# Kernel tuning notes

Measured on AMD Instinct MI355X. Metric: run time of the kernel, lower is better.

The kernel has to match this reference:

```python
import jax, jax.numpy as jnp
import numpy as np

ITEM_NUM = 50000
TARGET_ITEM_NUM = 50000
EMB = 128
N_LAYERS = 3
N_EDGES = 800000
N_NODES = ITEM_NUM + 1  # forward uses item_emb[:item_num+1]


def gcn_conv(x, row, col, W, b, n):
    """PyG GCNConv: symmetric-normalized aggregation with self-loops.
    out = D^{-1/2} (A + I) D^{-1/2} (x @ W) + b
    """
    h = x @ W  # [n, d]
    loops = jnp.arange(n)
    r = jnp.concatenate([row, loops])  # source
    c = jnp.concatenate([col, loops])  # target
    deg = jax.ops.segment_sum(jnp.ones(r.shape[0], x.dtype), c, num_segments=n)
    dinv = jnp.where(deg > 0, deg ** -0.5, jnp.zeros_like(deg))
    norm = dinv[r] * dinv[c]  # [E+n]
    out = jax.ops.segment_sum(h[r] * norm[:, None], c, num_segments=n)
    return out + b


def setup_inputs() -> dict:
    key = jax.random.key(0)
    k0, k1, k2 = jax.random.split(key, 3)
    edge_index = jax.random.randint(k0, (2, N_EDGES), 0, N_NODES)
    total = ITEM_NUM + TARGET_ITEM_NUM + 1
    # xavier_uniform for embedding table and per-layer GCN weights
    lim_e = float(np.sqrt(6.0 / (total + EMB)))
    item_emb = jax.random.uniform(k1, (total, EMB), jnp.float32, -lim_e, lim_e)
    lim_w = float(np.sqrt(6.0 / (EMB + EMB)))
    W = jax.random.uniform(k2, (N_LAYERS, EMB, EMB), jnp.float32, -lim_w, lim_w)
    b = jnp.zeros((N_LAYERS, EMB), jnp.float32)
    return {"edge_index": edge_index, "item_emb": item_emb, "W": W, "b": b}


def reference(edge_index, item_emb, W, b):
    n = N_NODES
    row, col = edge_index[0], edge_index[1]
    embeds = [item_emb[:n]]
    for i in range(N_LAYERS):
        embeds.append(gcn_conv(embeds[-1], row, col, W[i], b[i], n))
    return sum(embeds)  # [n, EMB], sum over layer embeddings
```

## Files before the change

### kernel.cpp

```cpp
#include <hip/hip_runtime.h>
#include <hip/hip_bf16.h>


constexpr int NN   = 50001;
constexpr int D    = 128;
constexpr int NPAD = 50048;
constexpr int NBK  = 196;
constexpr int CAP  = 7680;
constexpr int ZROW = NPAD - 1;

using bf16x8 = __attribute__((ext_vector_type(8))) short;
using f32x4  = __attribute__((ext_vector_type(4))) float;
using u16x8  = __attribute__((ext_vector_type(8))) unsigned short;
using u32x4  = __attribute__((ext_vector_type(4))) unsigned;

__device__ __forceinline__ ushort f2b(float f) {
    unsigned u = __float_as_uint(f);
    return (ushort)((u + 0x7FFFu + ((u >> 16) & 1u)) >> 16);
}
__device__ __forceinline__ float b2f(ushort u) {
    return __uint_as_float((unsigned)u << 16);
}

__global__ __launch_bounds__(256)
void k_build(const int* __restrict__ row, const int* __restrict__ col,
             int* __restrict__ partCur, unsigned* __restrict__ part,
             const float* __restrict__ W, ushort* __restrict__ Wt, int E) {
    int b = blockIdx.x, t = threadIdx.x;
    if (b < NBK) {
        __shared__ int hist[256];
        __shared__ int base[256];
        hist[t] = 0;
        __syncthreads();
        int e0 = b * 4096;
        unsigned rec[16];
        int bkt[16];
#pragma unroll
        for (int k = 0; k < 16; k++) {
            int e = e0 + k * 256 + t;
            if (e < E) {
                int r = row[e], c = col[e];
                rec[k] = (unsigned)r | ((unsigned)(c & 255) << 16);
                bkt[k] = c >> 8;
                atomicAdd(&hist[bkt[k]], 1);
            } else bkt[k] = -1;
        }
        __syncthreads();
        if (hist[t] > 0) base[t] = t * CAP + atomicAdd(&partCur[t], hist[t]);
        __syncthreads();
#pragma unroll
        for (int k = 0; k < 16; k++) {
            if (bkt[k] >= 0) {
                int pos = atomicAdd(&base[bkt[k]], 1);
                if (pos < (bkt[k] + 1) * CAP) part[pos] = rec[k];
            }
        }
    } else {
        int idx = (b - NBK) * 256 + t;
        int l = idx >> 14, rem = idx & 16383;
        int c = rem >> 7, k = rem & 127;
        Wt[idx] = f2b(W[l * D * D + k * D + c]);
    }
}

__global__ __launch_bounds__(256)
void k_scat(const unsigned* __restrict__ part, const int* __restrict__ partCur,
            float* __restrict__ dinv, unsigned* __restrict__ rp,
            ushort* __restrict__ meta, int n) {
    __shared__ int hist[256];
    __shared__ int sm[256];
    __shared__ int off[256];
    __shared__ int cur[256];
    int b = blockIdx.x, t = threadIdx.x;
    int node0 = b * 256;
    int nn = min(256, n - node0);
    int T = min(partCur[b], CAP);
    const unsigned* pb = part + (size_t)b * CAP;
    hist[t] = 0;
    __syncthreads();
    for (int i = t; i < T; i += 256) atomicAdd(&hist[pb[i] >> 16], 1);
    __syncthreads();
    int v = hist[t];
    int pv = (v + 15) & ~15;
    sm[t] = pv;
    __syncthreads();
    for (int ofs = 1; ofs < 256; ofs <<= 1) {
        int u = (t >= ofs) ? sm[t - ofs] : 0;
        __syncthreads();
        sm[t] += u;
        __syncthreads();
    }
    off[t] = sm[t] - pv;
    cur[t] = 0;
    if (t < nn) {
        dinv[node0 + t] = rsqrtf((float)v + 1.0f);
        rp[node0 + t] = (unsigned)(b * CAP + off[t]) | ((unsigned)v << 21);
    }
    __syncthreads();
    for (int i = t; i < T; i += 256) {
        unsigned rec = pb[i];
        int dl = (int)(rec >> 16);
        int pos = off[dl] + atomicAdd(&cur[dl], 1);
        if (pos < CAP) meta[(size_t)b * CAP + pos] = (ushort)(rec & 0xFFFFu);
    }
    int base = off[t];
    for (int p = v; p < pv; p++)
        if (base + p < CAP) meta[(size_t)b * CAP + base + p] = (ushort)ZROW;
}

constexpr int WT_LD = 136;
__global__ __launch_bounds__(256)
void k_gemm0(const float* __restrict__ emb, const ushort* __restrict__ WtL,
             const float* __restrict__ dinv, ushort* __restrict__ h, int n) {
    __shared__ ushort wlds[D * WT_LD];
    for (int idx = threadIdx.x; idx < D * (D / 8); idx += 256) {
        int r = idx >> 4, c8 = (idx & 15) * 8;
        *(uint4*)&wlds[r * WT_LD + c8] = *(const uint4*)&WtL[r * D + c8];
    }
    __syncthreads();

    int wave = threadIdx.x >> 6, lane = threadIdx.x & 63;
    int q = lane >> 4, i = lane & 15;
    int waveRow = blockIdx.x * 128 + wave * 32;

    bf16x8 a[2][4];
#pragma unroll
    for (int rt = 0; rt < 2; rt++) {
        const float* base = emb + (size_t)(waveRow + rt * 16 + i) * D + q * 8;
#pragma unroll
        for (int ks = 0; ks < 4; ks++) {
            float4 v0 = *(const float4*)(base + ks * 32);
            float4 v1 = *(const float4*)(base + ks * 32 + 4);
            bf16x8 aa;
            aa[0] = (short)f2b(v0.x); aa[1] = (short)f2b(v0.y);
            aa[2] = (short)f2b(v0.z); aa[3] = (short)f2b(v0.w);
            aa[4] = (short)f2b(v1.x); aa[5] = (short)f2b(v1.y);
            aa[6] = (short)f2b(v1.z); aa[7] = (short)f2b(v1.w);
            a[rt][ks] = aa;
        }
    }

    f32x4 acc[2][8] = {};
#pragma unroll
    for (int ct = 0; ct < 8; ct++) {
        const ushort* wbase = &wlds[(ct * 16 + i) * WT_LD + q * 8];
#pragma unroll
        for (int ks = 0; ks < 4; ks++) {
            bf16x8 bfr = *(const bf16x8*)(wbase + ks * 32);
            acc[0][ct] = __builtin_amdgcn_mfma_f32_16x16x32_bf16(a[0][ks], bfr, acc[0][ct], 0, 0, 0);
            acc[1][ct] = __builtin_amdgcn_mfma_f32_16x16x32_bf16(a[1][ks], bfr, acc[1][ct], 0, 0, 0);
        }
    }

#pragma unroll
    for (int rt = 0; rt < 2; rt++)
#pragma unroll
        for (int r4 = 0; r4 < 4; r4++) {
            int row = waveRow + rt * 16 + q * 4 + r4;
            float dv = (row < n) ? dinv[row] : 0.f;
#pragma unroll
            for (int ct = 0; ct < 8; ct++)
                h[(size_t)row * D + ct * 16 + i] = f2b(acc[rt][ct][r4] * dv);
        }
}

__global__ __launch_bounds__(256)
void k_fused(const unsigned* __restrict__ rp, const ushort* __restrict__ meta,
             const ushort* __restrict__ h_in,
             const float* __restrict__ dinv, const float* __restrict__ bias,
             const ushort* __restrict__ Wn,
             ushort* __restrict__ xb_out, ushort* __restrict__ h_out, int n) {
    __shared__ ushort xlds[16 * WT_LD];
    __shared__ float  sdinv[16];
    int tid  = threadIdx.x;
    int nl   = tid >> 4;
    int l    = tid & 15;
    int node0 = blockIdx.x * 16;
    int node  = node0 + nl;

    u16x8 w = {0, 0, 0, 0, 0, 0, 0, 0};
    float di = 0.f;
    if (node < n) {
        unsigned pk = rp[node];
        int s   = (int)(pk & 0x1FFFFFu);
        int deg = (int)(pk >> 21);
        const ushort* hl = h_in + (l << 3);

        u32x4 sv = *(const u32x4*)(hl + (size_t)node * D);
        di = dinv[node];
        const float4* bp = (const float4*)(bias + (l << 3));
        float4 b0 = bp[0], b1 = bp[1];

        float accL[4], accH[4];
#pragma unroll
        for (int k = 0; k < 4; k++) {
            accL[k] = __uint_as_float(sv[k] << 16);
            accH[k] = __uint_as_float(sv[k] & 0xFFFF0000u);
        }
        for (int j = 0; j < deg; j += 16) {
            u16x8 m0 = *(const u16x8*)&meta[s + j];
            u16x8 m1 = *(const u16x8*)&meta[s + j + 8];
            u32x4 v[16];
#pragma unroll
            for (int u = 0; u < 8; u++) v[u]     = *(const u32x4*)(hl + (size_t)m0[u] * D);
#pragma unroll
            for (int u = 0; u < 8; u++) v[8 + u] = *(const u32x4*)(hl + (size_t)m1[u] * D);
#pragma unroll
            for (int u = 0; u < 16; u++)
#pragma unroll
                for (int k = 0; k < 4; k++) {
                    accL[k] += __uint_as_float(v[u][k] << 16);
                    accH[k] += __uint_as_float(v[u][k] & 0xFFFF0000u);
                }
        }
        w[0] = f2b(fmaf(accL[0], di, b0.x));
        w[1] = f2b(fmaf(accH[0], di, b0.y));
        w[2] = f2b(fmaf(accL[1], di, b0.z));
        w[3] = f2b(fmaf(accH[1], di, b0.w));
        w[4] = f2b(fmaf(accL[2], di, b1.x));
        w[5] = f2b(fmaf(accH[2], di, b1.y));
        w[6] = f2b(fmaf(accL[3], di, b1.z));
        w[7] = f2b(fmaf(accH[3], di, b1.w));
        *(u16x8*)(xb_out + (size_t)node * D + (l << 3)) = w;
    }
    *(u16x8*)&xlds[nl * WT_LD + l * 8] = w;
    if (l == 0) sdinv[nl] = di;
    __syncthreads();

    int wave = tid >> 6, lane = tid & 63;
    int q = lane >> 4, i = lane & 15;

    bf16x8 a[4];
#pragma unroll
    for (int ks = 0; ks < 4; ks++)
        a[ks] = *(const bf16x8*)&xlds[i * WT_LD + ks * 32 + q * 8];

    f32x4 acc[2] = {};
#pragma unroll
    for (int ct = 0; ct < 2; ct++) {
        const ushort* wbase = &Wn[(size_t)(wave * 32 + ct * 16 + i) * D + q * 8];
#pragma unroll
        for (int ks = 0; ks < 4; ks++) {
            bf16x8 bfr = *(const bf16x8*)(wbase + ks * 32);
            acc[ct] = __builtin_amdgcn_mfma_f32_16x16x32_bf16(a[ks], bfr, acc[ct], 0, 0, 0);
        }
    }

#pragma unroll
    for (int r4 = 0; r4 < 4; r4++) {
        int rr = q * 4 + r4;
        float dv = sdinv[rr];
#pragma unroll
        for (int ct = 0; ct < 2; ct++)
            h_out[(size_t)(node0 + rr) * D + wave * 32 + ct * 16 + i] =
                f2b(acc[ct][r4] * dv);
    }
}

__global__ __launch_bounds__(256)
void k_pull_final(const unsigned* __restrict__ rp, const ushort* __restrict__ meta,
                  const ushort* __restrict__ h,
                  const float* __restrict__ dinv, const float* __restrict__ bias,
                  const float* __restrict__ emb, const ushort* __restrict__ x1,
                  const ushort* __restrict__ x2, float* __restrict__ out, int n) {
    int node = blockIdx.x * 16 + (threadIdx.x >> 4);
    int l    = threadIdx.x & 15;
    if (node >= n) return;
    unsigned pk = rp[node];
    int s   = (int)(pk & 0x1FFFFFu);
    int deg = (int)(pk >> 21);
    size_t o = (size_t)node * D + (l << 3);
    const ushort* hl = h + (l << 3);

    u32x4 sv = *(const u32x4*)(hl + (size_t)node * D);
    float di = dinv[node];
    const float4* bp = (const float4*)(bias + (l << 3));
    float4 b0 = bp[0], b1 = bp[1];
    const float4* ep = (const float4*)(emb + o);
    float4 e0 = ep[0], e1 = ep[1];
    u16x8 w1 = *(const u16x8*)(x1 + o);
    u16x8 w2 = *(const u16x8*)(x2 + o);

    float accL[4], accH[4];
#pragma unroll
    for (int k = 0; k < 4; k++) {
        accL[k] = __uint_as_float(sv[k] << 16);
        accH[k] = __uint_as_float(sv[k] & 0xFFFF0000u);
    }
    for (int j = 0; j < deg; j += 16) {
        u16x8 m0 = *(const u16x8*)&meta[s + j];
        u16x8 m1 = *(const u16x8*)&meta[s + j + 8];
        u32x4 v[16];
#pragma unroll
        for (int u = 0; u < 8; u++) v[u]     = *(const u32x4*)(hl + (size_t)m0[u] * D);
#pragma unroll
        for (int u = 0; u < 8; u++) v[8 + u] = *(const u32x4*)(hl + (size_t)m1[u] * D);
#pragma unroll
        for (int u = 0; u < 16; u++)
#pragma unroll
            for (int k = 0; k < 4; k++) {
                accL[k] += __uint_as_float(v[u][k] << 16);
                accH[k] += __uint_as_float(v[u][k] & 0xFFFF0000u);
            }
    }
    f32x4 o0, o1;
    o0[0] = e0.x + b2f(w1[0]) + b2f(w2[0]) + fmaf(accL[0], di, b0.x);
    o0[1] = e0.y + b2f(w1[1]) + b2f(w2[1]) + fmaf(accH[0], di, b0.y);
    o0[2] = e0.z + b2f(w1[2]) + b2f(w2[2]) + fmaf(accL[1], di, b0.z);
    o0[3] = e0.w + b2f(w1[3]) + b2f(w2[3]) + fmaf(accH[1], di, b0.w);
    o1[0] = e1.x + b2f(w1[4]) + b2f(w2[4]) + fmaf(accL[2], di, b1.x);
    o1[1] = e1.y + b2f(w1[5]) + b2f(w2[5]) + fmaf(accH[2], di, b1.y);
    o1[2] = e1.z + b2f(w1[6]) + b2f(w2[6]) + fmaf(accL[3], di, b1.z);
    o1[3] = e1.w + b2f(w1[7]) + b2f(w2[7]) + fmaf(accH[3], di, b1.w);
    __builtin_nontemporal_store(o0, (f32x4*)(out + o));
    __builtin_nontemporal_store(o1, (f32x4*)(out + o) + 1);
}

extern "C" void kernel_launch(void* const* d_in, const int* in_sizes, int n_in,
                              void* d_out, int out_size, void* d_ws, size_t ws_size,
                              hipStream_t stream) {
    const int*   edge = (const int*)d_in[0];
    const float* emb  = (const float*)d_in[1];
    const float* W    = (const float*)d_in[2];
    const float* b    = (const float*)d_in[3];
    float* out = (float*)d_out;

    const int E = in_sizes[0] / 2;
    const int n = NN;
    const int* row = edge;
    const int* col = edge + E;

    char* ws = (char*)d_ws;
    size_t off = 0;
    auto carve = [&](size_t bytes) { char* p = ws + off; off = (off + bytes + 511) / 512 * 512; return p; };
    int*      partCur = (int*)     carve(256 * 4);
    unsigned* part    = (unsigned*)carve((size_t)NBK * CAP * 4);
    ushort*   meta    = (ushort*)  carve((size_t)NBK * CAP * 2);
    unsigned* rp      = (unsigned*)carve((size_t)n * 4);
    float*    dinv    = (float*)   carve((size_t)n * 4);
    ushort*   Wt      = (ushort*)  carve((size_t)3 * D * D * 2);
    ushort*   xb1     = (ushort*)  carve((size_t)NPAD * D * 2);
    ushort*   xb2     = (ushort*)  carve((size_t)NPAD * D * 2);
    ushort*   hA      = (ushort*)  carve((size_t)NPAD * D * 2);
    ushort*   hB      = (ushort*)  carve((size_t)NPAD * D * 2);

    (void)hipMemsetAsync(partCur, 0, 256 * 4, stream);

    const int build_blocks = NBK + 192;
    k_build<<<build_blocks, 256, 0, stream>>>(row, col, partCur, part, W, Wt, E);
    k_scat <<<NBK, 256, 0, stream>>>(part, partCur, dinv, rp, meta, n);

    const int gemm_blocks  = NPAD / 128;
    const int fused_blocks = NPAD / 16;
    const int final_blocks = (n + 15) / 16;

    k_gemm0<<<gemm_blocks, 256, 0, stream>>>(emb, Wt, dinv, hA, n);
    k_fused<<<fused_blocks, 256, 0, stream>>>(rp, meta, hA, dinv, b,
                                              Wt + (size_t)1 * D * D, xb1, hB, n);
    k_fused<<<fused_blocks, 256, 0, stream>>>(rp, meta, hB, dinv, b + D,
                                              Wt + (size_t)2 * D * D, xb2, hA, n);
    k_pull_final<<<final_blocks, 256, 0, stream>>>(rp, meta, hA, dinv, b + 2 * D,
                                                   emb, xb1, xb2, out, n);
}
```

Baseline: 243.0 us.

## Fold layer-0 GEMM into the graph-build kernel and move dinv scaling into gather

The first-layer GEMM (emb @ W0) no longer depends on dinv, so it now runs inside the edge-bucketing prep kernel as extra blocks, which removes one launch and lets the GEMM overlap with the partitioning. Layer 1's aggregation therefore scales each gathered neighbour row by its dinv (an extra per-edge dinv load and FMA), and the self term is scaled by di. dinv is padded to NPAD with zeros so ZROW padding indices stay valid. The cost is extra random dinv reads in the first fused pass and a larger shared-memory footprint in the prep kernel.

```diff
diff --git a/kernel.cpp b/kernel.cpp
--- a/kernel.cpp
+++ b/kernel.cpp
@@ -8,6 +8,7 @@
 constexpr int NBK  = 196;
 constexpr int CAP  = 7680;
 constexpr int ZROW = NPAD - 1;
+constexpr int GB   = NPAD / 128;
 
 using bf16x8 = __attribute__((ext_vector_type(8))) short;
 using f32x4  = __attribute__((ext_vector_type(4))) float;
@@ -22,17 +23,77 @@
     return __uint_as_float((unsigned)u << 16);
 }
 
+constexpr int WT_LD = 136;
+
 __global__ __launch_bounds__(256)
-void k_build(const int* __restrict__ row, const int* __restrict__ col,
-             int* __restrict__ partCur, unsigned* __restrict__ part,
-             const float* __restrict__ W, ushort* __restrict__ Wt, int E) {
+void k_prep(const int* __restrict__ row, const int* __restrict__ col,
+            int* __restrict__ partCur, unsigned* __restrict__ part,
+            const float* __restrict__ W, ushort* __restrict__ Wt,
+            const float* __restrict__ emb, ushort* __restrict__ h,
+            int E, int n) {
+    __shared__ ushort wlds[D * WT_LD];
     int b = blockIdx.x, t = threadIdx.x;
-    if (b < NBK) {
-        __shared__ int hist[256];
-        __shared__ int base[256];
+
+    if (b < GB) {
+        for (int i4 = t; i4 < D * (D / 4); i4 += 256) {
+            int k = i4 >> 5, c4 = (i4 & 31) * 4;
+            float4 v = ((const float4*)W)[i4];
+            wlds[(c4 + 0) * WT_LD + k] = f2b(v.x);
+            wlds[(c4 + 1) * WT_LD + k] = f2b(v.y);
+            wlds[(c4 + 2) * WT_LD + k] = f2b(v.z);
+            wlds[(c4 + 3) * WT_LD + k] = f2b(v.w);
+        }
+        __syncthreads();
+
+        int wave = t >> 6, lane = t & 63;
+        int q = lane >> 4, i = lane & 15;
+        int waveRow = b * 128 + wave * 32;
+
+        bf16x8 a[2][4];
+#pragma unroll
+        for (int rt = 0; rt < 2; rt++) {
+            const float* base = emb + (size_t)(waveRow + rt * 16 + i) * D + q * 8;
+#pragma unroll
+            for (int ks = 0; ks < 4; ks++) {
+                float4 v0 = *(const float4*)(base + ks * 32);
+                float4 v1 = *(const float4*)(base + ks * 32 + 4);
+                bf16x8 aa;
+                aa[0] = (short)f2b(v0.x); aa[1] = (short)f2b(v0.y);
+                aa[2] = (short)f2b(v0.z); aa[3] = (short)f2b(v0.w);
+                aa[4] = (short)f2b(v1.x); aa[5] = (short)f2b(v1.y);
+                aa[6] = (short)f2b(v1.z); aa[7] = (short)f2b(v1.w);
+                a[rt][ks] = aa;
+            }
+        }
+
+        f32x4 acc[2][8] = {};
+#pragma unroll
+        for (int ct = 0; ct < 8; ct++) {
+            const ushort* wbase = &wlds[(ct * 16 + i) * WT_LD + q * 8];
+#pragma unroll
+            for (int ks = 0; ks < 4; ks++) {
+                bf16x8 bfr = *(const bf16x8*)(wbase + ks * 32);
+                acc[0][ct] = __builtin_amdgcn_mfma_f32_16x16x32_bf16(a[0][ks], bfr, acc[0][ct], 0, 0, 0);
+                acc[1][ct] = __builtin_amdgcn_mfma_f32_16x16x32_bf16(a[1][ks], bfr, acc[1][ct], 0, 0, 0);
+            }
+        }
+
+#pragma unroll
+        for (int rt = 0; rt < 2; rt++)
+#pragma unroll
+            for (int r4 = 0; r4 < 4; r4++) {
+                int r = waveRow + rt * 16 + q * 4 + r4;
+#pragma unroll
+                for (int ct = 0; ct < 8; ct++)
+                    h[(size_t)r * D + ct * 16 + i] =
+                        (r < n) ? f2b(acc[rt][ct][r4]) : (ushort)0;
+            }
+    } else if (b < GB + NBK) {
+        int* hist = (int*)wlds;
+        int* base = hist + 256;
         hist[t] = 0;
         __syncthreads();
-        int e0 = b * 4096;
+        int e0 = (b - GB) * 4096;
         unsigned rec[16];
         int bkt[16];
 #pragma unroll
@@ -56,10 +117,10 @@
             }
         }
     } else {
-        int idx = (b - NBK) * 256 + t;
-        int l = idx >> 14, rem = idx & 16383;
+        int idx = (b - GB - NBK) * 256 + t;
+        int l = 1 + (idx >> 14), rem = idx & 16383;
         int c = rem >> 7, k = rem & 127;
-        Wt[idx] = f2b(W[l * D * D + k * D + c]);
+        Wt[(size_t)16384 + idx] = f2b(W[l * D * D + k * D + c]);
     }
 }
 
@@ -95,6 +156,8 @@
     if (t < nn) {
         dinv[node0 + t] = rsqrtf((float)v + 1.0f);
         rp[node0 + t] = (unsigned)(b * CAP + off[t]) | ((unsigned)v << 21);
+    } else if (node0 + t < NPAD) {
+        dinv[node0 + t] = 0.f;
     }
     __syncthreads();
     for (int i = t; i < T; i += 256) {
@@ -108,62 +171,7 @@
         if (base + p < CAP) meta[(size_t)b * CAP + base + p] = (ushort)ZROW;
 }
 
-constexpr int WT_LD = 136;
-__global__ __launch_bounds__(256)
-void k_gemm0(const float* __restrict__ emb, const ushort* __restrict__ WtL,
-             const float* __restrict__ dinv, ushort* __restrict__ h, int n) {
-    __shared__ ushort wlds[D * WT_LD];
-    for (int idx = threadIdx.x; idx < D * (D / 8); idx += 256) {
-        int r = idx >> 4, c8 = (idx & 15) * 8;
-        *(uint4*)&wlds[r * WT_LD + c8] = *(const uint4*)&WtL[r * D + c8];
-    }
-    __syncthreads();
-
-    int wave = threadIdx.x >> 6, lane = threadIdx.x & 63;
-    int q = lane >> 4, i = lane & 15;
-    int waveRow = blockIdx.x * 128 + wave * 32;
-
-    bf16x8 a[2][4];
-#pragma unroll
-    for (int rt = 0; rt < 2; rt++) {
-        const float* base = emb + (size_t)(waveRow + rt * 16 + i) * D + q * 8;
-#pragma unroll
-        for (int ks = 0; ks < 4; ks++) {
-            float4 v0 = *(const float4*)(base + ks * 32);
-            float4 v1 = *(const float4*)(base + ks * 32 + 4);
-            bf16x8 aa;
-            aa[0] = (short)f2b(v0.x); aa[1] = (short)f2b(v0.y);
-            aa[2] = (short)f2b(v0.z); aa[3] = (short)f2b(v0.w);
-            aa[4] = (short)f2b(v1.x); aa[5] = (short)f2b(v1.y);
-            aa[6] = (short)f2b(v1.z); aa[7] = (short)f2b(v1.w);
-            a[rt][ks] = aa;
-        }
-    }
-
-    f32x4 acc[2][8] = {};
-#pragma unroll
-    for (int ct = 0; ct < 8; ct++) {
-        const ushort* wbase = &wlds[(ct * 16 + i) * WT_LD + q * 8];
-#pragma unroll
-        for (int ks = 0; ks < 4; ks++) {
-            bf16x8 bfr = *(const bf16x8*)(wbase + ks * 32);
-            acc[0][ct] = __builtin_amdgcn_mfma_f32_16x16x32_bf16(a[0][ks], bfr, acc[0][ct], 0, 0, 0);
-            acc[1][ct] = __builtin_amdgcn_mfma_f32_16x16x32_bf16(a[1][ks], bfr, acc[1][ct], 0, 0, 0);
-        }
-    }
-
-#pragma unroll
-    for (int rt = 0; rt < 2; rt++)
-#pragma unroll
-        for (int r4 = 0; r4 < 4; r4++) {
-            int row = waveRow + rt * 16 + q * 4 + r4;
-            float dv = (row < n) ? dinv[row] : 0.f;
-#pragma unroll
-            for (int ct = 0; ct < 8; ct++)
-                h[(size_t)row * D + ct * 16 + i] = f2b(acc[rt][ct][r4] * dv);
-        }
-}
-
+template <int SCALED>
 __global__ __launch_bounds__(256)
 void k_fused(const unsigned* __restrict__ rp, const ushort* __restrict__ meta,
              const ushort* __restrict__ h_in,
@@ -191,11 +199,12 @@
         const float4* bp = (const float4*)(bias + (l << 3));
         float4 b0 = bp[0], b1 = bp[1];
 
+        float selfs = SCALED ? 1.f : di;
         float accL[4], accH[4];
 #pragma unroll
         for (int k = 0; k < 4; k++) {
-            accL[k] = __uint_as_float(sv[k] << 16);
-            accH[k] = __uint_as_float(sv[k] & 0xFFFF0000u);
+            accL[k] = selfs * __uint_as_float(sv[k] << 16);
+            accH[k] = selfs * __uint_as_float(sv[k] & 0xFFFF0000u);
         }
         for (int j = 0; j < deg; j += 16) {
             u16x8 m0 = *(const u16x8*)&meta[s + j];
@@ -205,12 +214,20 @@
             for (int u = 0; u < 8; u++) v[u]     = *(const u32x4*)(hl + (size_t)m0[u] * D);
 #pragma unroll
             for (int u = 0; u < 8; u++) v[8 + u] = *(const u32x4*)(hl + (size_t)m1[u] * D);
+            float dv[16];
+            if constexpr (!SCALED) {
+#pragma unroll
+                for (int u = 0; u < 8; u++) { dv[u] = dinv[m0[u]]; dv[8 + u] = dinv[m1[u]]; }
+            }
 #pragma unroll
             for (int u = 0; u < 16; u++)
 #pragma unroll
                 for (int k = 0; k < 4; k++) {
-                    accL[k] += __uint_as_float(v[u][k] << 16);
-                    accH[k] += __uint_as_float(v[u][k] & 0xFFFF0000u);
+                    float lo = __uint_as_float(v[u][k] << 16);
+                    float hi = __uint_as_float(v[u][k] & 0xFFFF0000u);
+                    if constexpr (SCALED) { accL[k] += lo; accH[k] += hi; }
+                    else { accL[k] = fmaf(lo, dv[u], accL[k]);
+                           accH[k] = fmaf(hi, dv[u], accH[k]); }
                 }
         }
         w[0] = f2b(fmaf(accL[0], di, b0.x));
@@ -337,7 +354,7 @@
     unsigned* part    = (unsigned*)carve((size_t)NBK * CAP * 4);
     ushort*   meta    = (ushort*)  carve((size_t)NBK * CAP * 2);
     unsigned* rp      = (unsigned*)carve((size_t)n * 4);
-    float*    dinv    = (float*)   carve((size_t)n * 4);
+    float*    dinv    = (float*)   carve((size_t)NPAD * 4);
     ushort*   Wt      = (ushort*)  carve((size_t)3 * D * D * 2);
     ushort*   xb1     = (ushort*)  carve((size_t)NPAD * D * 2);
     ushort*   xb2     = (ushort*)  carve((size_t)NPAD * D * 2);
@@ -346,19 +363,17 @@
 
     (void)hipMemsetAsync(partCur, 0, 256 * 4, stream);
 
-    const int build_blocks = NBK + 192;
-    k_build<<<build_blocks, 256, 0, stream>>>(row, col, partCur, part, W, Wt, E);
-    k_scat <<<NBK, 256, 0, stream>>>(part, partCur, dinv, rp, meta, n);
-
-    const int gemm_blocks  = NPAD / 128;
+    const int prep_blocks  = GB + NBK + 128;
+    k_prep<<<prep_blocks, 256, 0, stream>>>(row, col, partCur, part, W, Wt, emb, hA, E, n);
+    k_scat<<<NBK, 256, 0, stream>>>(part, partCur, dinv, rp, meta, n);
+
     const int fused_blocks = NPAD / 16;
     const int final_blocks = (n + 15) / 16;
 
-    k_gemm0<<<gemm_blocks, 256, 0, stream>>>(emb, Wt, dinv, hA, n);
-    k_fused<<<fused_blocks, 256, 0, stream>>>(rp, meta, hA, dinv, b,
-                                              Wt + (size_t)1 * D * D, xb1, hB, n);
-    k_fused<<<fused_blocks, 256, 0, stream>>>(rp, meta, hB, dinv, b + D,
-                                              Wt + (size_t)2 * D * D, xb2, hA, n);
+    k_fused<0><<<fused_blocks, 256, 0, stream>>>(rp, meta, hA, dinv, b,
+                                                 Wt + (size_t)1 * D * D, xb1, hB, n);
+    k_fused<1><<<fused_blocks, 256, 0, stream>>>(rp, meta, hB, dinv, b + D,
+                                                 Wt + (size_t)2 * D * D, xb2, hA, n);
     k_pull_final<<<final_blocks, 256, 0, stream>>>(rp, meta, hA, dinv, b + 2 * D,
                                                    emb, xb1, xb2, out, n);
 }
```

Result: slower. 256.1 us (+5.4%).
